# Performance work log

Measured on AMD Instinct MI355X. Metric: run time of the kernel, lower is better.

Reference implementation:

```python
import jax, jax.numpy as jnp
import numpy as np

D = 512      # feature dim d
N = 8192     # context length n
LMBD = 0.9   # eligibility trace decay


def _build_consts():
    two_d1 = 2 * D + 1
    # P: single nonzero entry at bottom-right
    P = np.zeros((two_d1, two_d1), dtype=np.float32)
    P[-1, -1] = 1.0
    # M: (n+1)x(n+1); top-left n x n block is lower-triangular lmbd^(row-col),
    # last row and last column are all zero (M[-1,-1] set to 0 in torch code)
    i = np.arange(N)
    diff = i[:, None] - i[None, :]
    Mnn = np.where(diff >= 0, LMBD ** np.maximum(diff, 0), 0.0).astype(np.float32)
    M = np.zeros((N + 1, N + 1), dtype=np.float32)
    M[:N, :N] = Mnn
    # Q: top-left 2d x 2d block = [[-I, I], [0, 0]]
    I = np.eye(D, dtype=np.float32)
    Q = np.zeros((two_d1, two_d1), dtype=np.float32)
    Q[:D, :D] = -I
    Q[:D, D:2 * D] = I
    return jnp.asarray(P), jnp.asarray(M), jnp.asarray(Q)


def setup_inputs() -> dict:
    key = jax.random.key(0)
    kz, = jax.random.split(key, 1)
    Z = jax.random.normal(kz, (2 * D + 1, N + 1), dtype=jnp.float32)
    alpha = jnp.ones((1,), dtype=jnp.float32)  # learned parameter
    P, M, Q = _build_consts()
    return {"Z": Z, "alpha": alpha, "P": P, "M": M, "Q": Q}


def reference(Z, alpha, P, M, Q):
    # Z: (2d+1, n+1). Matches torch: Z + alpha/n * P @ Z @ M @ Z.T @ Q @ Z
    n = Z.shape[1] - 1
    upd = ((((P @ Z) @ M) @ Z.T) @ Q) @ Z  # left-to-right like torch's @ chain
    return Z + (alpha[0] / n) * upd
```

## Files before the change

kernel.cpp:

```cpp
#include <hip/hip_runtime.h>

#define ND   512
#define NN   8192
#define NP1  8193
#define NCHUNK 32

typedef float f4 __attribute__((ext_vector_type(4)));

__global__ void k1_v_hicopy(const float* __restrict__ Z, float* __restrict__ v,
                            float* __restrict__ out) {
    int b = blockIdx.x;
    if (b < 129) {
        int tid = threadIdx.x;
        int jj = b * 64 + (tid >> 2);
        if (jj > NN) return;
        int p = tid & 3;
        if (jj == NN) { if (p == 0) v[jj] = 0.0f; return; }
        const float* z = Z + (size_t)(2 * ND) * NP1;
        const float l1 = 0.9f;
        const float l2 = l1 * l1, l4 = l2 * l2, l8 = l4 * l4;
        const float l16 = l8 * l8, l32 = l16 * l16, l48 = l32 * l16;
        float scale = (p == 0) ? 1.0f
                    : (p == 1) ? l48
                    : (p == 2) ? l48 * l48
                               : l48 * l48 * l48;
        int base = jj + 48 * p;
        float p0 = scale, p1 = scale * l1, p2 = scale * l2, p3 = scale * l2 * l1;
        float a0 = 0.f, a1 = 0.f, a2 = 0.f, a3 = 0.f;
#pragma unroll
        for (int m = 0; m < 48; m += 4) {
            int i = base + m;
            float z0 = (i     < NN) ? z[i]     : 0.0f;
            float z1 = (i + 1 < NN) ? z[i + 1] : 0.0f;
            float z2 = (i + 2 < NN) ? z[i + 2] : 0.0f;
            float z3 = (i + 3 < NN) ? z[i + 3] : 0.0f;
            a0 = fmaf(p0, z0, a0);
            a1 = fmaf(p1, z1, a1);
            a2 = fmaf(p2, z2, a2);
            a3 = fmaf(p3, z3, a3);
            p0 *= l4; p1 *= l4; p2 *= l4; p3 *= l4;
        }
        float a = (a0 + a2) + (a1 + a3);
        a += __shfl_xor(a, 1, 64);
        a += __shfl_xor(a, 2, 64);
        if (p == 0) v[jj] = a;
    } else {
        const f4* src = (const f4*)Z + 1048704u;
        f4*       dst = (f4*)out     + 1048704u;
        const unsigned STR = 895u * 256u;
        unsigned i = (unsigned)(b - 129) * 256u + threadIdx.x;
        while (i + STR < 1048704u) {
            f4 x0 = src[i];
            f4 x1 = src[i + STR];
            __builtin_nontemporal_store(x0, &dst[i]);
            __builtin_nontemporal_store(x1, &dst[i + STR]);
            i += 2u * STR;
        }
        if (i < 1048704u) {
            f4 x0 = src[i];
            __builtin_nontemporal_store(x0, &dst[i]);
        }
    }
}

__global__ __launch_bounds__(1024) void k2_wcopy(const float* __restrict__ Z,
                                                 const float* __restrict__ v,
                                                 float* __restrict__ w,
                                                 float* __restrict__ out) {
    int c = blockIdx.x;
    const float* row = Z + (size_t)c * NP1;
    float* orow = out + (size_t)c * NP1;
    int t = threadIdx.x;
    float r0 = row[t        ], r1 = row[t + 1024 ], r2 = row[t + 2048 ], r3 = row[t + 3072 ];
    float r4 = row[t + 4096 ], r5 = row[t + 5120 ], r6 = row[t + 6144 ], r7 = row[t + 7168 ];
    __builtin_nontemporal_store(r0, &orow[t        ]);
    __builtin_nontemporal_store(r1, &orow[t + 1024 ]);
    __builtin_nontemporal_store(r2, &orow[t + 2048 ]);
    __builtin_nontemporal_store(r3, &orow[t + 3072 ]);
    __builtin_nontemporal_store(r4, &orow[t + 4096 ]);
    __builtin_nontemporal_store(r5, &orow[t + 5120 ]);
    __builtin_nontemporal_store(r6, &orow[t + 6144 ]);
    __builtin_nontemporal_store(r7, &orow[t + 7168 ]);
    if (t == 0) orow[NN] = row[NN];
    float acc = 0.f;
    acc = fmaf(r0, v[t        ], acc);
    acc = fmaf(r1, v[t + 1024 ], acc);
    acc = fmaf(r2, v[t + 2048 ], acc);
    acc = fmaf(r3, v[t + 3072 ], acc);
    acc = fmaf(r4, v[t + 4096 ], acc);
    acc = fmaf(r5, v[t + 5120 ], acc);
    acc = fmaf(r6, v[t + 6144 ], acc);
    acc = fmaf(r7, v[t + 7168 ], acc);
    for (int off = 32; off > 0; off >>= 1)
        acc += __shfl_down(acc, off, 64);
    __shared__ float red[16];
    if ((t & 63) == 0) red[t >> 6] = acc;
    __syncthreads();
    if (t == 0) {
        float s = 0.f;
#pragma unroll
        for (int k = 0; k < 16; ++k) s += red[k];
        w[c] = s;
    }
}

__global__ void k3_u(const float* __restrict__ Z, const float* __restrict__ w,
                     float* __restrict__ upart) {
    int j = blockIdx.x * 256 + threadIdx.x;
    if (j >= NP1) return;
    int c0 = blockIdx.y * 16;
    const size_t DS = (size_t)ND * NP1;
    float acc0 = 0.f, acc1 = 0.f;
#pragma unroll
    for (int cb = 0; cb < 16; cb += 4) {
        size_t b0 = (size_t)(c0 + cb) * NP1 + j;
        size_t b1 = b0 + NP1;
        size_t b2 = b1 + NP1;
        size_t b3 = b2 + NP1;
        float lo0 = Z[b0], lo1 = Z[b1], lo2 = Z[b2], lo3 = Z[b3];
        float hi0 = Z[b0 + DS], hi1 = Z[b1 + DS], hi2 = Z[b2 + DS], hi3 = Z[b3 + DS];
        acc0 = fmaf(w[c0 + cb    ], hi0 - lo0, acc0);
        acc1 = fmaf(w[c0 + cb + 1], hi1 - lo1, acc1);
        acc0 = fmaf(w[c0 + cb + 2], hi2 - lo2, acc0);
        acc1 = fmaf(w[c0 + cb + 3], hi3 - lo3, acc1);
    }
    upart[(size_t)blockIdx.y * NP1 + j] = acc0 + acc1;
}

__global__ void k4_fin(const float* __restrict__ Z, const float* __restrict__ upart,
                       const float* __restrict__ alpha, float* __restrict__ out) {
    int gid = blockIdx.x * 256 + threadIdx.x;
    int j = gid >> 2;
    if (j >= NP1) return;
    int p = gid & 3;
    float u = 0.f;
#pragma unroll
    for (int k = p * 8; k < p * 8 + 8; ++k)
        u += upart[(size_t)k * NP1 + j];
    u += __shfl_xor(u, 1, 64);
    u += __shfl_xor(u, 2, 64);
    if (p == 0) {
        float s = alpha[0] / (float)NN;
        const size_t off = (size_t)(2 * ND) * NP1 + j;
        out[off] = fmaf(s, u, Z[off]);
    }
}

extern "C" void kernel_launch(void* const* d_in, const int* in_sizes, int n_in,
                              void* d_out, int out_size, void* d_ws, size_t ws_size,
                              hipStream_t stream) {
    const float* Z     = (const float*)d_in[0];
    const float* alpha = (const float*)d_in[1];
    float* out = (float*)d_out;

    float* v     = (float*)d_ws;
    float* w     = v + NP1;
    float* upart = w + ND;

    k1_v_hicopy<<<1024, 256, 0, stream>>>(Z, v, out);
    k2_wcopy<<<ND, 1024, 0, stream>>>(Z, v, w, out);
    dim3 gu((NP1 + 255) / 256, NCHUNK);
    k3_u<<<gu, 256, 0, stream>>>(Z, w, upart);
    k4_fin<<<(4 * NP1 + 255) / 256, 256, 0, stream>>>(Z, upart, alpha, out);
}
```

Measured before the change: 27.31 us.

## Move full output copy into first kernel, make w kernel read-only

The bulk copy of Z into out moves out of the w-reduction kernel and into the first kernel, which now launches 2050 copy blocks that each move four float4 elements with a fixed stride. The copy covers the whole array instead of only the top half, and one block handles the tail. k2 becomes a pure dot-product reduction with eight independent accumulators. Launch bounds are added to the other kernels. The aim is to run the copy alongside the v computation and lighten k2, at the cost of a much larger first kernel that may delay v and so k2.

After: 28.03 us. 1.03x slower.

```diff
diff --git a/kernel.cpp b/kernel.cpp
--- a/kernel.cpp
+++ b/kernel.cpp
@@ -7,12 +7,18 @@
 
 typedef float f4 __attribute__((ext_vector_type(4)));
 
-__global__ void k1_v_hicopy(const float* __restrict__ Z, float* __restrict__ v,
-                            float* __restrict__ out) {
-    int b = blockIdx.x;
-    if (b < 129) {
+#define NF4    2099456u
+#define NVBLK  129u
+#define NCPB   2050u
+#define CSTR   524800u
+
+__global__ __launch_bounds__(256) void k1_v_copy(const float* __restrict__ Z,
+                                                 float* __restrict__ v,
+                                                 float* __restrict__ out) {
+    unsigned b = blockIdx.x;
+    if (b < NVBLK) {
         int tid = threadIdx.x;
-        int jj = b * 64 + (tid >> 2);
+        int jj = (int)b * 64 + (tid >> 2);
         if (jj > NN) return;
         int p = tid & 3;
         if (jj == NN) { if (p == 0) v[jj] = 0.0f; return; }
@@ -45,52 +51,44 @@
         a += __shfl_xor(a, 2, 64);
         if (p == 0) v[jj] = a;
     } else {
-        const f4* src = (const f4*)Z + 1048704u;
-        f4*       dst = (f4*)out     + 1048704u;
-        const unsigned STR = 895u * 256u;
-        unsigned i = (unsigned)(b - 129) * 256u + threadIdx.x;
-        while (i + STR < 1048704u) {
-            f4 x0 = src[i];
-            f4 x1 = src[i + STR];
-            __builtin_nontemporal_store(x0, &dst[i]);
-            __builtin_nontemporal_store(x1, &dst[i + STR]);
-            i += 2u * STR;
-        }
-        if (i < 1048704u) {
-            f4 x0 = src[i];
-            __builtin_nontemporal_store(x0, &dst[i]);
+        unsigned cb = b - NVBLK;
+        const f4* __restrict__ src = (const f4*)Z;
+        f4* __restrict__ dst = (f4*)out;
+        unsigned i = cb * 256u + threadIdx.x;
+        f4 x0 = src[i];
+        f4 x1 = src[i +      CSTR];
+        f4 x2 = src[i + 2u * CSTR];
+        f4 x3 = src[i + 3u * CSTR];
+        __builtin_nontemporal_store(x0, &dst[i]);
+        __builtin_nontemporal_store(x1, &dst[i +      CSTR]);
+        __builtin_nontemporal_store(x2, &dst[i + 2u * CSTR]);
+        __builtin_nontemporal_store(x3, &dst[i + 3u * CSTR]);
+        if (cb == 0u) {
+            unsigned j = 2099200u + threadIdx.x;
+            f4 y = src[j];
+            __builtin_nontemporal_store(y, &dst[j]);
+            if (threadIdx.x == 0u) out[8397824u] = Z[8397824u];
         }
     }
 }
 
-__global__ __launch_bounds__(1024) void k2_wcopy(const float* __restrict__ Z,
-                                                 const float* __restrict__ v,
-                                                 float* __restrict__ w,
-                                                 float* __restrict__ out) {
+__global__ __launch_bounds__(1024) void k2_w(const float* __restrict__ Z,
+                                             const float* __restrict__ v,
+                                             float* __restrict__ w) {
     int c = blockIdx.x;
     const float* row = Z + (size_t)c * NP1;
-    float* orow = out + (size_t)c * NP1;
     int t = threadIdx.x;
-    float r0 = row[t        ], r1 = row[t + 1024 ], r2 = row[t + 2048 ], r3 = row[t + 3072 ];
-    float r4 = row[t + 4096 ], r5 = row[t + 5120 ], r6 = row[t + 6144 ], r7 = row[t + 7168 ];
-    __builtin_nontemporal_store(r0, &orow[t        ]);
-    __builtin_nontemporal_store(r1, &orow[t + 1024 ]);
-    __builtin_nontemporal_store(r2, &orow[t + 2048 ]);
-    __builtin_nontemporal_store(r3, &orow[t + 3072 ]);
-    __builtin_nontemporal_store(r4, &orow[t + 4096 ]);
-    __builtin_nontemporal_store(r5, &orow[t + 5120 ]);
-    __builtin_nontemporal_store(r6, &orow[t + 6144 ]);
-    __builtin_nontemporal_store(r7, &orow[t + 7168 ]);
-    if (t == 0) orow[NN] = row[NN];
-    float acc = 0.f;
-    acc = fmaf(r0, v[t        ], acc);
-    acc = fmaf(r1, v[t + 1024 ], acc);
-    acc = fmaf(r2, v[t + 2048 ], acc);
-    acc = fmaf(r3, v[t + 3072 ], acc);
-    acc = fmaf(r4, v[t + 4096 ], acc);
-    acc = fmaf(r5, v[t + 5120 ], acc);
-    acc = fmaf(r6, v[t + 6144 ], acc);
-    acc = fmaf(r7, v[t + 7168 ], acc);
+    float a0 = 0.f, a1 = 0.f, a2 = 0.f, a3 = 0.f;
+    float a4 = 0.f, a5 = 0.f, a6 = 0.f, a7 = 0.f;
+    a0 = fmaf(row[t        ], v[t        ], a0);
+    a1 = fmaf(row[t + 1024 ], v[t + 1024 ], a1);
+    a2 = fmaf(row[t + 2048 ], v[t + 2048 ], a2);
+    a3 = fmaf(row[t + 3072 ], v[t + 3072 ], a3);
+    a4 = fmaf(row[t + 4096 ], v[t + 4096 ], a4);
+    a5 = fmaf(row[t + 5120 ], v[t + 5120 ], a5);
+    a6 = fmaf(row[t + 6144 ], v[t + 6144 ], a6);
+    a7 = fmaf(row[t + 7168 ], v[t + 7168 ], a7);
+    float acc = ((a0 + a1) + (a2 + a3)) + ((a4 + a5) + (a6 + a7));
     for (int off = 32; off > 0; off >>= 1)
         acc += __shfl_down(acc, off, 64);
     __shared__ float red[16];
@@ -104,8 +102,9 @@
     }
 }
 
-__global__ void k3_u(const float* __restrict__ Z, const float* __restrict__ w,
-                     float* __restrict__ upart) {
+__global__ __launch_bounds__(256) void k3_u(const float* __restrict__ Z,
+                                            const float* __restrict__ w,
+                                            float* __restrict__ upart) {
     int j = blockIdx.x * 256 + threadIdx.x;
     if (j >= NP1) return;
     int c0 = blockIdx.y * 16;
@@ -127,8 +126,10 @@
     upart[(size_t)blockIdx.y * NP1 + j] = acc0 + acc1;
 }
 
-__global__ void k4_fin(const float* __restrict__ Z, const float* __restrict__ upart,
-                       const float* __restrict__ alpha, float* __restrict__ out) {
+__global__ __launch_bounds__(256) void k4_fin(const float* __restrict__ Z,
+                                              const float* __restrict__ upart,
+                                              const float* __restrict__ alpha,
+                                              float* __restrict__ out) {
     int gid = blockIdx.x * 256 + threadIdx.x;
     int j = gid >> 2;
     if (j >= NP1) return;
@@ -157,8 +158,8 @@
     float* w     = v + NP1;
     float* upart = w + ND;
 
-    k1_v_hicopy<<<1024, 256, 0, stream>>>(Z, v, out);
-    k2_wcopy<<<ND, 1024, 0, stream>>>(Z, v, w, out);
+    k1_v_copy<<<NVBLK + NCPB, 256, 0, stream>>>(Z, v, out);
+    k2_w<<<ND, 1024, 0, stream>>>(Z, v, w);
     dim3 gu((NP1 + 255) / 256, NCHUNK);
     k3_u<<<gu, 256, 0, stream>>>(Z, w, upart);
     k4_fin<<<(4 * NP1 + 255) / 256, 256, 0, stream>>>(Z, upart, alpha, out);
```
